# Optimization experiments

Hardware: AMD Instinct MI355X
Metric: run time of the kernel (lower is better)

## Reference

```python
import jax, jax.numpy as jnp
import numpy as np

H = 8  # n_head
EPS = 1e-5


def layernorm(x, g, b):
    m = jnp.mean(x, -1, keepdims=True)
    v = jnp.mean((x - m) ** 2, -1, keepdims=True)
    return (x - m) * jax.lax.rsqrt(v + EPS) * g + b


def setup_inputs() -> dict:
    key = jax.random.key(0)
    ks = jax.random.split(key, 32)
    b, t, d, f, n_mem, l_mem = 4, 256, 512, 2048, 64, 128
    sd = 1.0 / np.sqrt(d)
    sf = 1.0 / np.sqrt(f)
    rn = lambda k, shape, s: jax.random.normal(k, shape, jnp.float32) * s
    inp = {
        'dec_output': rn(ks[0], (b, t, d), 1.0),
        'tgt_mask': jnp.ones((b, t), dtype=bool),
        'mem_attn_out': rn(ks[1], (b, t, n_mem + 1), 1.0),
        'enc_out_mem': rn(ks[2], (n_mem, l_mem, d), 1.0),
        'tgt_emb_mem': rn(ks[3], (n_mem, l_mem, d), 1.0),
        'tgt_mask_mem': jnp.ones((n_mem, l_mem), dtype=bool),
        # MultiHeadedAttention params
        'Wq': rn(ks[4], (d, d), sd), 'bq': jnp.zeros((d,)),
        'Wk': rn(ks[5], (d, d), sd), 'bk': jnp.zeros((d,)),
        'Wv': rn(ks[6], (d, d), sd), 'bv': jnp.zeros((d,)),
        'Wo': rn(ks[7], (d, d), sd), 'bo': jnp.zeros((d,)),
        # LayerNorms (norms[0] pre, norms[1] post)
        'g0': jnp.ones((d,)), 'be0': jnp.zeros((d,)),
        'g1': jnp.ones((d,)), 'be1': jnp.zeros((d,)),
        # pos_ffn (applied to attended tokens)
        'W1': rn(ks[8], (d, f), sd), 'bf1': jnp.zeros((f,)),
        'W2': rn(ks[9], (f, d), sf), 'bf2': jnp.zeros((d,)),
        # pos_ffn2 (applied to all tokens at the end)
        'W3': rn(ks[10], (d, f), sd), 'bf3': jnp.zeros((f,)),
        'W4': rn(ks[11], (f, d), sf), 'bf4': jnp.zeros((d,)),
    }
    return inp


def reference(dec_output, tgt_mask, mem_attn_out, enc_out_mem, tgt_emb_mem, tgt_mask_mem,
              Wq, bq, Wk, bk, Wv, bv, Wo, bo, g0, be0, g1, be1,
              W1, bf1, W2, bf2, W3, bf3, W4, bf4):
    b, t, d = dec_output.shape
    dh = d // H
    x = layernorm(dec_output, g0, be0)                       # norms[0]

    samples = jnp.argmax(mem_attn_out, -1) - 1               # [b,t], -1 => no memory
    valid = samples >= 0
    s = jnp.clip(samples, 0, None)                           # safe gather index

    # Per-token gather of the selected memory entry (irregular access).
    K = enc_out_mem[s]                                       # [b,t,l_mem,d]
    V = tgt_emb_mem[s]                                       # [b,t,l_mem,d]
    kmask = tgt_mask_mem[s]                                  # [b,t,l_mem] True=valid

    # Single-row attention: token (b,t) queries memory entry samples[b,t].
    q = (x @ Wq + bq).reshape(b, t, H, dh)
    k = (K @ Wk + bk).reshape(b, t, -1, H, dh)
    v = (V @ Wv + bv).reshape(b, t, -1, H, dh)
    scores = jnp.einsum('bthd,btlhd->bthl', q, k) / np.sqrt(dh)
    scores = jnp.where(kmask[:, :, None, :], scores, -1e9)
    attn = jax.nn.softmax(scores, axis=-1)
    ctx = jnp.einsum('bthl,btlhd->bthd', attn, v).reshape(b, t, d)
    st = ctx @ Wo + bo + x                                   # residual = query

    # pos_ffn (residual) then norms[1]
    st = st + jax.nn.relu(st @ W1 + bf1) @ W2 + bf2
    st = layernorm(st, g1, be1)

    # scatter-back: zero for tokens with sample == -1
    x = x + jnp.where(valid[..., None], st, 0.0)

    # pos_ffn2 (residual)
    out = x + jax.nn.relu(x @ W3 + bf3) @ W4 + bf4
    return out
```

## Files before the change

kernel.cpp:

```cpp
#include <hip/hip_runtime.h>
#include <hip/hip_bf16.h>
#include <math.h>

#define DD    512
#define FF    2048
#define NMEM  64
#define LMEM  128
#define NH    8
#define DH    64
#define NTOK  1024
#define NMROW 8192

typedef __attribute__((ext_vector_type(4))) float f32x4;
typedef __attribute__((ext_vector_type(8))) short bf16x8;

__device__ inline unsigned short f2b(float f) {
    union { float f; unsigned int i; } u; u.f = f;
    unsigned int r = u.i + 0x7FFFu + ((u.i >> 16) & 1u);
    return (unsigned short)(r >> 16);
}
__device__ inline float b2f(unsigned short b) {
    union { unsigned int i; float f; } u; u.i = ((unsigned int)b) << 16;
    return u.f;
}
__device__ __forceinline__ void gload_lds(const void* src, void* dst) {
    __builtin_amdgcn_global_load_lds((const __attribute__((address_space(1))) void*)src,
        (__attribute__((address_space(3))) void*)dst, 16, 0, 0);
}

struct WSeg { const float* src; unsigned short* dst; int K, N, tile0; };

struct PrepArgs {
    const float4 *enc, *emb; ushort4 *encb, *embb;
    WSeg s[3];
    const float *mem_attn;
    int *samples, *blist, *bstart;
    const float *dec, *g0, *be0;
    float *x; unsigned short *xb, *ctxb;
};

__global__ __launch_bounds__(256)
void prep_kernel(PrepArgs a) {
    __shared__ float ld[32][33];
    __shared__ float red[8];
    __shared__ int ibuf[64 + 65 + 64];
    int b = blockIdx.x, tid = threadIdx.x;
    if (b < 4096) {
        int i = b * 256 + tid;
        float4 va = a.enc[i];
        a.encb[i] = make_ushort4(f2b(va.x), f2b(va.y), f2b(va.z), f2b(va.w));
        float4 vb = a.emb[i];
        a.embb[i] = make_ushort4(f2b(vb.x), f2b(vb.y), f2b(vb.z), f2b(vb.w));
        return;
    }
    if (b < 4864) {
        int t = b - 4096;
        int si = 0;
#pragma unroll
        for (int i = 1; i < 3; ++i) if (t >= a.s[i].tile0) si = i;
        const float* src = a.s[si].src;
        unsigned short* dst = a.s[si].dst;
        int K = a.s[si].K, N = a.s[si].N;
        int lt = t - a.s[si].tile0;
        int ntn = N >> 5;
        int k0 = (lt / ntn) << 5, n0 = (lt % ntn) << 5;
        int r = tid >> 3, c = (tid & 7) << 2;
        float4 v = *(const float4*)(src + (size_t)(k0 + r) * N + n0 + c);
        ld[r][c] = v.x; ld[r][c + 1] = v.y; ld[r][c + 2] = v.z; ld[r][c + 3] = v.w;
        __syncthreads();
        ushort4 o = make_ushort4(f2b(ld[c][r]), f2b(ld[c + 1][r]),
                                 f2b(ld[c + 2][r]), f2b(ld[c + 3][r]));
        *(ushort4*)(dst + (size_t)(n0 + r) * K + k0 + c) = o;
        return;
    }
    if (b < 5888) {
        int row = b - 4864;
        const float* xr = a.dec + (size_t)row * DD;
        float v0 = xr[tid], v1 = xr[tid + 256];
        float s = v0 + v1, s2 = v0 * v0 + v1 * v1;
        for (int off = 32; off > 0; off >>= 1) {
            s  += __shfl_down(s,  off, 64);
            s2 += __shfl_down(s2, off, 64);
        }
        int wave = tid >> 6, lane = tid & 63;
        if (lane == 0) { red[wave] = s; red[4 + wave] = s2; }
        __syncthreads();
        float S  = red[0] + red[1] + red[2] + red[3];
        float S2 = red[4] + red[5] + red[6] + red[7];
        float mean = S / (float)DD;
        float inv  = rsqrtf(S2 / (float)DD - mean * mean + 1e-5f);
        float o0 = (v0 - mean) * inv * a.g0[tid]       + a.be0[tid];
        float o1 = (v1 - mean) * inv * a.g0[tid + 256] + a.be0[tid + 256];
        size_t base = (size_t)row * DD;
        a.x[base + tid] = o0; a.x[base + tid + 256] = o1;
        a.xb[base + tid] = f2b(o0); a.xb[base + tid + 256] = f2b(o1);
        ((unsigned*)a.ctxb)[row * 256 + tid] = 0u;
        return;
    }
    int* scnt  = ibuf;
    int* soff  = ibuf + 64;
    int* scnt2 = ibuf + 129;
    if (tid < 64) { scnt[tid] = 0; scnt2[tid] = 0; }
    __syncthreads();
    int mys[4];
#pragma unroll
    for (int k = 0; k < 4; ++k) {
        int t = k * 256 + tid;
        const float* r = a.mem_attn + (size_t)t * (NMEM + 1);
        float best = r[0]; int bi = 0;
        for (int i = 1; i < NMEM + 1; ++i) {
            float v = r[i];
            if (v > best) { best = v; bi = i; }
        }
        int s = bi - 1;
        a.samples[t] = s; mys[k] = s;
        if (s >= 0) atomicAdd(&scnt[s], 1);
    }
    __syncthreads();
    if (tid == 0) {
        int run = 0;
        for (int e = 0; e < 64; ++e) { soff[e] = run; run += scnt[e]; }
        soff[64] = run;
    }
    __syncthreads();
    if (tid < 65) a.bstart[tid] = soff[tid];
#pragma unroll
    for (int k = 0; k < 4; ++k) {
        int t = k * 256 + tid;
        int s = mys[k];
        if (s >= 0) {
            int pos = soff[s] + atomicAdd(&scnt2[s], 1);
            a.blist[pos] = t;
        }
    }
}

__global__ __launch_bounds__(256)
void ln_scatter_kernel(const float* __restrict__ st2, const float* __restrict__ g,
                       const float* __restrict__ be, const float* __restrict__ x,
                       const int* __restrict__ samples, float* __restrict__ x2,
                       unsigned short* __restrict__ x2b) {
    int row = blockIdx.x;
    const float* xr = st2 + (size_t)row * DD;
    int tid = threadIdx.x;
    float v0 = xr[tid], v1 = xr[tid + 256];
    float s = v0 + v1, s2 = v0 * v0 + v1 * v1;
    for (int off = 32; off > 0; off >>= 1) {
        s  += __shfl_down(s,  off, 64);
        s2 += __shfl_down(s2, off, 64);
    }
    __shared__ float red[8];
    int wave = tid >> 6, lane = tid & 63;
    if (lane == 0) { red[wave] = s; red[4 + wave] = s2; }
    __syncthreads();
    float S  = red[0] + red[1] + red[2] + red[3];
    float S2 = red[4] + red[5] + red[6] + red[7];
    float mean = S / (float)DD;
    float inv  = rsqrtf(S2 / (float)DD - mean * mean + 1e-5f);
    float valid = (samples[row] >= 0) ? 1.f : 0.f;
    size_t base = (size_t)row * DD;
    float l0 = (v0 - mean) * inv * g[tid]       + be[tid];
    float l1 = (v1 - mean) * inv * g[tid + 256] + be[tid + 256];
    float r0 = x[base + tid]       + valid * l0;
    float r1 = x[base + tid + 256] + valid * l1;
    x2[base + tid] = r0; x2[base + tid + 256] = r1;
    x2b[base + tid] = f2b(r0); x2b[base + tid + 256] = f2b(r1);
}

template<int MI, int NI, int BK>
__device__ __forceinline__
void gemm_core(const unsigned short* __restrict__ A, const unsigned short* __restrict__ Bt,
               const float* __restrict__ bias, const float* __restrict__ res,
               float* __restrict__ C, unsigned short* __restrict__ Cb,
               int N, int K, int relu, int bx, int by,
               unsigned short* As0, unsigned short* As1,
               unsigned short* Bs0, unsigned short* Bs1) {
    constexpr int BM = MI * 32, BN = NI * 32;
    constexpr int CPR = BK / 8;
    constexpr int RB  = BK * 2;
    static_assert((BM * CPR + BN * CPR) / 256 == 8 || BK == 512, "8 loads/wave/tile");
    const int tid = threadIdx.x;
    const int lane = tid & 63, w = tid >> 6;
    const int wm = (w >> 1) * (MI * 16), wn = (w & 1) * (NI * 16);
    const int m0 = by * BM, n0 = bx * BN;
    f32x4 acc[MI][NI] = {};

    auto stage = [&](unsigned short* As, unsigned short* Bs, int k0) {
#pragma unroll
        for (int it = 0; it < BM * CPR / 256; ++it) {
            int f = it * 256 + tid;
            int row = f / CPR, ch = f % CPR;
            int sch = ch ^ (row & 7);
            gload_lds((const char*)(A + (size_t)(m0 + row) * K + k0) + sch * 16,
                      (char*)As + f * 16);
        }
#pragma unroll
        for (int it = 0; it < BN * CPR / 256; ++it) {
            int f = it * 256 + tid;
            int row = f / CPR, ch = f % CPR;
            int sch = ch ^ (row & 7);
            gload_lds((const char*)(Bt + (size_t)(n0 + row) * K + k0) + sch * 16,
                      (char*)Bs + f * 16);
        }
    };

    const int nt = K / BK;
    stage(As0, Bs0, 0);
    if (nt > 1) stage(As1, Bs1, BK);
    for (int t = 0; t < nt; ++t) {
        if (t + 1 < nt) {
            asm volatile("s_waitcnt vmcnt(8)" ::: "memory");
        } else {
            asm volatile("s_waitcnt vmcnt(0)" ::: "memory");
        }
        __builtin_amdgcn_s_barrier();
        __builtin_amdgcn_sched_barrier(0);
        const unsigned short* As = (t & 1) ? As1 : As0;
        const unsigned short* Bs = (t & 1) ? Bs1 : Bs0;
#pragma unroll
        for (int kk = 0; kk < BK / 32; ++kk) {
            bf16x8 af[MI], bfr[NI];
#pragma unroll
            for (int mi = 0; mi < MI; ++mi) {
                int row = wm + mi * 16 + (lane & 15);
                int ch = kk * 4 + (lane >> 4);
                af[mi] = *(const bf16x8*)((const char*)As + row * RB + ((ch ^ (row & 7)) * 16));
            }
#pragma unroll
            for (int ni = 0; ni < NI; ++ni) {
                int row = wn + ni * 16 + (lane & 15);
                int ch = kk * 4 + (lane >> 4);
                bfr[ni] = *(const bf16x8*)((const char*)Bs + row * RB + ((ch ^ (row & 7)) * 16));
            }
#pragma unroll
            for (int mi = 0; mi < MI; ++mi)
#pragma unroll
                for (int ni = 0; ni < NI; ++ni)
                    acc[mi][ni] = __builtin_amdgcn_mfma_f32_16x16x32_bf16(af[mi], bfr[ni], acc[mi][ni], 0, 0, 0);
        }
        __builtin_amdgcn_s_barrier();
        if (t + 2 < nt)
            stage((t & 1) ? As1 : As0, (t & 1) ? Bs1 : Bs0, (t + 2) * BK);
    }
#pragma unroll
    for (int mi = 0; mi < MI; ++mi) {
#pragma unroll
        for (int ni = 0; ni < NI; ++ni) {
            int col = n0 + wn + ni * 16 + (lane & 15);
            float bv = bias[col];
#pragma unroll
            for (int j = 0; j < 4; ++j) {
                int row = m0 + wm + mi * 16 + (lane >> 4) * 4 + j;
                size_t idx = (size_t)row * N + col;
                float v = acc[mi][ni][j] + bv;
                if (res)  v += res[idx];
                if (relu) v = fmaxf(v, 0.f);
                if (C)  C[idx] = v;
                if (Cb) Cb[idx] = f2b(v);
            }
        }
    }
}

template<int MI, int NI, int BK, int RELU>
__global__ __launch_bounds__(256)
void gemm_kernel(const unsigned short* __restrict__ A, const unsigned short* __restrict__ Bt,
                 const float* __restrict__ bias, const float* __restrict__ res,
                 float* __restrict__ C, unsigned short* __restrict__ Cb, int N, int K) {
    __shared__ __align__(16) unsigned short As0[MI * 32 * BK], As1[MI * 32 * BK];
    __shared__ __align__(16) unsigned short Bs0[NI * 32 * BK], Bs1[NI * 32 * BK];
    gemm_core<MI, NI, BK>(A, Bt, bias, res, C, Cb, N, K, RELU, blockIdx.x, blockIdx.y,
                          As0, As1, Bs0, Bs1);
}

template<int MI, int NI, int BK, int RELU>
__global__ __launch_bounds__(256)
void gemm1_kernel(const unsigned short* __restrict__ A, const unsigned short* __restrict__ Bt,
                  const float* __restrict__ bias, const float* __restrict__ res,
                  float* __restrict__ C, unsigned short* __restrict__ Cb, int N) {
    __shared__ __align__(16) unsigned short As[MI * 32 * BK];
    __shared__ __align__(16) unsigned short Bs[NI * 32 * BK];
    gemm_core<MI, NI, BK>(A, Bt, bias, res, C, Cb, N, BK, RELU, blockIdx.x, blockIdx.y,
                          As, As, Bs, Bs);
}

struct WSeg5s { WSeg s[5]; };

__global__ __launch_bounds__(256)
void attn_fused_kernel(const unsigned short* __restrict__ encb,
                       const unsigned short* __restrict__ embb,
                       const unsigned short* __restrict__ xb,
                       const unsigned short* __restrict__ WkT,
                       const unsigned short* __restrict__ WvT,
                       const unsigned short* __restrict__ WqT,
                       const float* __restrict__ bk, const float* __restrict__ bv,
                       const float* __restrict__ bq,
                       const int* __restrict__ blist, const int* __restrict__ bstart,
                       unsigned short* __restrict__ ctxb, WSeg5s wsegs) {
    __shared__ __align__(16) unsigned short As[128 * 64];
    __shared__ __align__(16) unsigned short Ws[64 * 64];
    __shared__ __align__(16) unsigned short Ks[128 * 64];
    __shared__ __align__(16) unsigned short Vt[64 * 128];
    __shared__ float qsb[32 * 64];
    __shared__ float ps[2][128];
    __shared__ float red[8];
    __shared__ int toks[32];
    const int b = blockIdx.x, tid = threadIdx.x;
    const int lane = tid & 63, w = tid >> 6;

    if (b >= 512) {
        float* ld = (float*)As;
#pragma unroll 1
        for (int j = 0; j < 8; ++j) {
            int t = (b - 512) * 8 + j;
            int si = 0;
#pragma unroll
            for (int i = 1; i < 5; ++i) if (t >= wsegs.s[i].tile0) si = i;
            const float* src = wsegs.s[si].src;
            unsigned short* dst = wsegs.s[si].dst;
            int K = wsegs.s[si].K, N = wsegs.s[si].N;
            int lt = t - wsegs.s[si].tile0;
            int ntn = N >> 5;
            int k0 = (lt / ntn) << 5, n0 = (lt % ntn) << 5;
            int r = tid >> 3, c = (tid & 7) << 2;
            float4 v = *(const float4*)(src + (size_t)(k0 + r) * N + n0 + c);
            ld[r * 33 + c] = v.x; ld[r * 33 + c + 1] = v.y;
            ld[r * 33 + c + 2] = v.z; ld[r * 33 + c + 3] = v.w;
            __syncthreads();
            ushort4 o = make_ushort4(f2b(ld[c * 33 + r]), f2b(ld[(c + 1) * 33 + r]),
                                     f2b(ld[(c + 2) * 33 + r]), f2b(ld[(c + 3) * 33 + r]));
            *(ushort4*)(dst + (size_t)(n0 + r) * K + k0 + c) = o;
            __syncthreads();
        }
        return;
    }

    const int e = b & 63, h = b >> 6;
    const int beg = bstart[e], end = bstart[e + 1];
    if (end <= beg) return;

#pragma unroll 1
    for (int ph = 0; ph < 2; ++ph) {
        const unsigned short* Am = (ph ? embb : encb) + (size_t)e * LMEM * DD;
        const unsigned short* Wm = (ph ? WvT : WkT) + (size_t)h * DH * DD;
        const float* bias = ph ? bv : bk;
        f32x4 acc[2][4] = {};
        for (int k0 = 0; k0 < DD; k0 += 64) {
            __syncthreads();
#pragma unroll
            for (int it = 0; it < 4; ++it) {
                int f = it * 256 + tid;
                int row = f >> 3, ch = f & 7, sch = ch ^ (row & 7);
                gload_lds((const char*)(Am + (size_t)row * DD + k0) + sch * 16,
                          (char*)As + f * 16);
            }
#pragma unroll
            for (int it = 0; it < 2; ++it) {
                int f = it * 256 + tid;
                int row = f >> 3, ch = f & 7, sch = ch ^ (row & 7);
                gload_lds((const char*)(Wm + (size_t)row * DD + k0) + sch * 16,
                          (char*)Ws + f * 16);
            }
            __syncthreads();
#pragma unroll
            for (int kk = 0; kk < 2; ++kk) {
                int ch = kk * 4 + (lane >> 4);
                bf16x8 af[2], bfr[4];
#pragma unroll
                for (int mi = 0; mi < 2; ++mi) {
                    int row = w * 32 + mi * 16 + (lane & 15);
                    af[mi] = *(const bf16x8*)((const char*)As + row * 128 + ((ch ^ (row & 7)) * 16));
                }
#pragma unroll
                for (int ni = 0; ni < 4; ++ni) {
                    int row = ni * 16 + (lane & 15);
                    bfr[ni] = *(const bf16x8*)((const char*)Ws + row * 128 + ((ch ^ (row & 7)) * 16));
                }
#pragma unroll
                for (int mi = 0; mi < 2; ++mi)
#pragma unroll
                    for (int ni = 0; ni < 4; ++ni)
                        acc[mi][ni] = __builtin_amdgcn_mfma_f32_16x16x32_bf16(af[mi], bfr[ni], acc[mi][ni], 0, 0, 0);
            }
        }
#pragma unroll
        for (int mi = 0; mi < 2; ++mi) {
#pragma unroll
            for (int ni = 0; ni < 4; ++ni) {
                int d = ni * 16 + (lane & 15);
                float bvv = bias[h * DH + d];
#pragma unroll
                for (int j = 0; j < 4; ++j) {
                    int l = w * 32 + mi * 16 + (lane >> 4) * 4 + j;
                    unsigned short val = f2b(acc[mi][ni][j] + bvv);
                    if (ph == 0) {
                        int c = d >> 3;
                        *(unsigned short*)((char*)Ks + l * 128 + ((c ^ (l & 7)) * 16) + (d & 7) * 2) = val;
                    } else {
                        int cc = l >> 3;
                        int slot = (cc & 8) | ((cc ^ d) & 7);
                        *(unsigned short*)((char*)Vt + d * 256 + slot * 16 + (l & 7) * 2) = val;
                    }
                }
            }
        }
    }

    const int sub = tid >> 7, lt = tid & 127;
    for (int g0 = beg; g0 < end; g0 += 32) {
        int gcnt = end - g0; if (gcnt > 32) gcnt = 32;
        __syncthreads();
        if (tid < 32) toks[tid] = blist[(g0 + tid < end) ? (g0 + tid) : (end - 1)];
        f32x4 qacc[2] = {};
        for (int k0 = 0; k0 < DD; k0 += 64) {
            __syncthreads();
            {
                int row = tid >> 3, ch = tid & 7, sch = ch ^ (row & 7);
                gload_lds((const char*)(xb + (size_t)toks[row] * DD + k0) + sch * 16,
                          (char*)As + tid * 16);
            }
#pragma unroll
            for (int it = 0; it < 2; ++it) {
                int f = it * 256 + tid;
                int row = f >> 3, ch = f & 7, sch = ch ^ (row & 7);
                gload_lds((const char*)(WqT + (size_t)(h * DH + row) * DD + k0) + sch * 16,
                          (char*)Ws + f * 16);
            }
            __syncthreads();
#pragma unroll
            for (int kk = 0; kk < 2; ++kk) {
                int ch = kk * 4 + (lane >> 4);
                int ar = (w >> 1) * 16 + (lane & 15);
                bf16x8 af = *(const bf16x8*)((const char*)As + ar * 128 + ((ch ^ (ar & 7)) * 16));
#pragma unroll
                for (int ni = 0; ni < 2; ++ni) {
                    int br = (w & 1) * 32 + ni * 16 + (lane & 15);
                    bf16x8 bfr = *(const bf16x8*)((const char*)Ws + br * 128 + ((ch ^ (br & 7)) * 16));
                    qacc[ni] = __builtin_amdgcn_mfma_f32_16x16x32_bf16(af, bfr, qacc[ni], 0, 0, 0);
                }
            }
        }
#pragma unroll
        for (int ni = 0; ni < 2; ++ni)
#pragma unroll
            for (int j = 0; j < 4; ++j) {
                int r = (w >> 1) * 16 + (lane >> 4) * 4 + j;
                int d = (w & 1) * 32 + ni * 16 + (lane & 15);
                qsb[r * 64 + d] = qacc[ni][j] + bq[h * DH + d];
            }
        __syncthreads();

        int iters = (gcnt + 1) >> 1;
        for (int it = 0; it < iters; ++it) {
            int tl = it * 2 + sub;
            float sc = 0.f;
#pragma unroll
            for (int c = 0; c < 8; ++c) {
                bf16x8 kv = *(const bf16x8*)((char*)Ks + lt * 128 + ((c ^ (lt & 7)) * 16));
#pragma unroll
                for (int j = 0; j < 8; ++j) sc = fmaf(qsb[tl * 64 + c * 8 + j], b2f((unsigned short)kv[j]), sc);
            }
            sc *= 0.125f;
            float mx = sc;
            for (int off = 32; off > 0; off >>= 1) mx = fmaxf(mx, __shfl_xor(mx, off, 64));
            if ((tid & 63) == 0) red[tid >> 6] = mx;
            __syncthreads();
            mx = fmaxf(red[sub * 2], red[sub * 2 + 1]);
            float ex = __expf(sc - mx);
            float sm = ex;
            for (int off = 32; off > 0; off >>= 1) sm += __shfl_xor(sm, off, 64);
            if ((tid & 63) == 0) red[4 + (tid >> 6)] = sm;
            __syncthreads();
            sm = red[4 + sub * 2] + red[4 + sub * 2 + 1];
            ps[sub][lt] = ex / sm;
            __syncthreads();
            if (tid < 128) {
                int sub2 = tid >> 6, d = tid & 63;
                int tl2 = it * 2 + sub2;
                if (g0 + tl2 < end) {
                    int tok2 = toks[tl2];
                    float acc2 = 0.f;
#pragma unroll
                    for (int cc = 0; cc < 16; ++cc) {
                        int slot = (cc & 8) | ((cc ^ d) & 7);
                        bf16x8 vv = *(const bf16x8*)((char*)Vt + d * 256 + slot * 16);
#pragma unroll
                        for (int j = 0; j < 8; ++j) acc2 = fmaf(ps[sub2][cc * 8 + j], b2f((unsigned short)vv[j]), acc2);
                    }
                    ctxb[(size_t)tok2 * DD + h * DH + d] = f2b(acc2);
                }
            }
            __syncthreads();
        }
    }
}

extern "C" void kernel_launch(void* const* d_in, const int* in_sizes, int n_in,
                              void* d_out, int out_size, void* d_ws, size_t ws_size,
                              hipStream_t stream) {
    const float* dec      = (const float*)d_in[0];
    const float* mem_attn = (const float*)d_in[2];
    const float* enc_mem  = (const float*)d_in[3];
    const float* emb_mem  = (const float*)d_in[4];
    const float* Wq = (const float*)d_in[6];  const float* bq = (const float*)d_in[7];
    const float* Wk = (const float*)d_in[8];  const float* bk = (const float*)d_in[9];
    const float* Wv = (const float*)d_in[10]; const float* bv = (const float*)d_in[11];
    const float* Wo = (const float*)d_in[12]; const float* bo = (const float*)d_in[13];
    const float* g0 = (const float*)d_in[14]; const float* be0 = (const float*)d_in[15];
    const float* g1 = (const float*)d_in[16]; const float* be1 = (const float*)d_in[17];
    const float* W1 = (const float*)d_in[18]; const float* bf1 = (const float*)d_in[19];
    const float* W2 = (const float*)d_in[20]; const float* bf2 = (const float*)d_in[21];
    const float* W3 = (const float*)d_in[22]; const float* bf3 = (const float*)d_in[23];
    const float* W4 = (const float*)d_in[24]; const float* bf4 = (const float*)d_in[25];
    float* out = (float*)d_out;

    const size_t MB = 1u << 20;
    char* ws = (char*)d_ws;
    unsigned short* encb  = (unsigned short*)(ws + 0 * MB);
    unsigned short* embb  = (unsigned short*)(ws + 8 * MB);
    unsigned short* WqT = (unsigned short*)(ws + 32 * MB);
    unsigned short* WkT = (unsigned short*)(ws + 32 * MB + 512 * 1024);
    unsigned short* WvT = (unsigned short*)(ws + 33 * MB);
    unsigned short* WoT = (unsigned short*)(ws + 33 * MB + 512 * 1024);
    unsigned short* W1T = (unsigned short*)(ws + 34 * MB);
    unsigned short* W2T = (unsigned short*)(ws + 36 * MB);
    unsigned short* W3T = (unsigned short*)(ws + 38 * MB);
    unsigned short* W4T = (unsigned short*)(ws + 40 * MB);
    float*          x    = (float*)(ws + 42 * MB);
    unsigned short* xb   = (unsigned short*)(ws + 44 * MB);
    unsigned short* ctxb = (unsigned short*)(ws + 47 * MB);
    int*         samples = (int*)(ws + 48 * MB);
    int*         blist   = (int*)(ws + 48 * MB + 4096);
    int*         bstart  = (int*)(ws + 48 * MB + 8192);
    float*          st   = (float*)(ws + 0 * MB);
    unsigned short* stb  = (unsigned short*)(ws + 2 * MB);
    unsigned short* h1b  = (unsigned short*)(ws + 3 * MB);
    float*          st2  = (float*)(ws + 8 * MB);
    float*          x2   = (float*)(ws + 10 * MB);
    unsigned short* x2b  = (unsigned short*)(ws + 12 * MB);
    unsigned short* h2b  = (unsigned short*)(ws + 13 * MB);

    PrepArgs pa;
    pa.enc = (const float4*)enc_mem; pa.emb = (const float4*)emb_mem;
    pa.encb = (ushort4*)encb; pa.embb = (ushort4*)embb;
    pa.s[0] = { Wq, WqT, DD, DD,   0 };
    pa.s[1] = { Wk, WkT, DD, DD, 256 };
    pa.s[2] = { Wv, WvT, DD, DD, 512 };
    pa.mem_attn = mem_attn; pa.samples = samples; pa.blist = blist; pa.bstart = bstart;
    pa.dec = dec; pa.g0 = g0; pa.be0 = be0;
    pa.x = x; pa.xb = xb; pa.ctxb = ctxb;
    prep_kernel<<<5889, 256, 0, stream>>>(pa);
    WSeg5s wt;
    wt.s[0] = { Wo, WoT, DD, DD,    0 };
    wt.s[1] = { W1, W1T, DD, FF,  256 };
    wt.s[2] = { W2, W2T, FF, DD, 1280 };
    wt.s[3] = { W3, W3T, DD, FF, 2304 };
    wt.s[4] = { W4, W4T, FF, DD, 3328 };
    attn_fused_kernel<<<512 + 544, 256, 0, stream>>>(encb, embb, xb, WkT, WvT, WqT,
                                                     bk, bv, bq, blist, bstart, ctxb, wt);
    gemm1_kernel<1,1,512,0><<<dim3(16, 32), 256, 0, stream>>>(ctxb, WoT, bo, x, st, stb, DD);
    gemm_kernel<2,2,128,1><<<dim3(32, 16), 256, 0, stream>>>(stb, W1T, bf1, nullptr, nullptr, h1b, FF, DD);
    gemm_kernel<1,1,256,0><<<dim3(16, 32), 256, 0, stream>>>(h1b, W2T, bf2, st, st2, nullptr, DD, FF);
    ln_scatter_kernel<<<NTOK, 256, 0, stream>>>(st2, g1, be1, x, samples, x2, x2b);
    gemm_kernel<2,2,128,1><<<dim3(32, 16), 256, 0, stream>>>(x2b, W3T, bf3, nullptr, nullptr, h2b, FF, DD);
    gemm_kernel<1,1,256,0><<<dim3(16, 32), 256, 0, stream>>>(h2b, W4T, bf4, x2, out, nullptr, DD, FF);
}
```

Baseline: 122.4 us.

## Use MFMA for memory attention scores and context, load K/V projection operands directly

Replaces the per-token scalar FMA score and context loops in the fused memory-attention kernel with bf16 MFMA tiles over 32 tokens at once, using a block-wide softmax reduction through shared memory. The K/V and Q projection GEMMs now read operands straight from global memory into registers instead of staging them through LDS, which frees shared memory. It also adds a launch-bounds occupancy hint. Scores and probabilities are rounded to bf16, which slightly reduces precision, and dropping LDS staging relies on the cache for operand reuse.

```diff
diff --git a/kernel.cpp b/kernel.cpp
--- a/kernel.cpp
+++ b/kernel.cpp
@@ -286,7 +286,7 @@
 
 struct WSeg5s { WSeg s[5]; };
 
-__global__ __launch_bounds__(256)
+__global__ __launch_bounds__(256, 3)
 void attn_fused_kernel(const unsigned short* __restrict__ encb,
                        const unsigned short* __restrict__ embb,
                        const unsigned short* __restrict__ xb,
@@ -297,19 +297,17 @@
                        const float* __restrict__ bq,
                        const int* __restrict__ blist, const int* __restrict__ bstart,
                        unsigned short* __restrict__ ctxb, WSeg5s wsegs) {
-    __shared__ __align__(16) unsigned short As[128 * 64];
-    __shared__ __align__(16) unsigned short Ws[64 * 64];
     __shared__ __align__(16) unsigned short Ks[128 * 64];
     __shared__ __align__(16) unsigned short Vt[64 * 128];
-    __shared__ float qsb[32 * 64];
-    __shared__ float ps[2][128];
-    __shared__ float red[8];
+    __shared__ __align__(16) unsigned short Qs[32 * 64];
+    __shared__ __align__(16) unsigned short Ps[32 * 128];
+    __shared__ float redm[2][32], reds[2][32];
     __shared__ int toks[32];
     const int b = blockIdx.x, tid = threadIdx.x;
     const int lane = tid & 63, w = tid >> 6;
 
     if (b >= 512) {
-        float* ld = (float*)As;
+        float* ld = (float*)Ks;
 #pragma unroll 1
         for (int j = 0; j < 8; ++j) {
             int t = (b - 512) * 8 + j;
@@ -341,47 +339,25 @@
 
 #pragma unroll 1
     for (int ph = 0; ph < 2; ++ph) {
-        const unsigned short* Am = (ph ? embb : encb) + (size_t)e * LMEM * DD;
-        const unsigned short* Wm = (ph ? WvT : WkT) + (size_t)h * DH * DD;
+        const unsigned short* Am = (ph ? embb : encb) + (size_t)e * (LMEM * DD);
+        const unsigned short* Wm = (ph ? WvT : WkT) + (size_t)h * (DH * DD);
         const float* bias = ph ? bv : bk;
         f32x4 acc[2][4] = {};
-        for (int k0 = 0; k0 < DD; k0 += 64) {
-            __syncthreads();
-#pragma unroll
-            for (int it = 0; it < 4; ++it) {
-                int f = it * 256 + tid;
-                int row = f >> 3, ch = f & 7, sch = ch ^ (row & 7);
-                gload_lds((const char*)(Am + (size_t)row * DD + k0) + sch * 16,
-                          (char*)As + f * 16);
-            }
-#pragma unroll
-            for (int it = 0; it < 2; ++it) {
-                int f = it * 256 + tid;
-                int row = f >> 3, ch = f & 7, sch = ch ^ (row & 7);
-                gload_lds((const char*)(Wm + (size_t)row * DD + k0) + sch * 16,
-                          (char*)Ws + f * 16);
-            }
-            __syncthreads();
-#pragma unroll
-            for (int kk = 0; kk < 2; ++kk) {
-                int ch = kk * 4 + (lane >> 4);
-                bf16x8 af[2], bfr[4];
-#pragma unroll
-                for (int mi = 0; mi < 2; ++mi) {
-                    int row = w * 32 + mi * 16 + (lane & 15);
-                    af[mi] = *(const bf16x8*)((const char*)As + row * 128 + ((ch ^ (row & 7)) * 16));
-                }
-#pragma unroll
-                for (int ni = 0; ni < 4; ++ni) {
-                    int row = ni * 16 + (lane & 15);
-                    bfr[ni] = *(const bf16x8*)((const char*)Ws + row * 128 + ((ch ^ (row & 7)) * 16));
-                }
-#pragma unroll
-                for (int mi = 0; mi < 2; ++mi)
-#pragma unroll
-                    for (int ni = 0; ni < 4; ++ni)
-                        acc[mi][ni] = __builtin_amdgcn_mfma_f32_16x16x32_bf16(af[mi], bfr[ni], acc[mi][ni], 0, 0, 0);
-            }
+        const unsigned short* ar0 = Am + (size_t)(w * 32 + (lane & 15)) * DD + (lane >> 4) * 8;
+        const unsigned short* br0 = Wm + (size_t)(lane & 15) * DD + (lane >> 4) * 8;
+#pragma unroll 4
+        for (int ks = 0; ks < 16; ++ks) {
+            bf16x8 af[2], bfr[4];
+            af[0] = *(const bf16x8*)(ar0 + ks * 32);
+            af[1] = *(const bf16x8*)(ar0 + 16 * DD + ks * 32);
+#pragma unroll
+            for (int ni = 0; ni < 4; ++ni)
+                bfr[ni] = *(const bf16x8*)(br0 + (size_t)ni * 16 * DD + ks * 32);
+#pragma unroll
+            for (int mi = 0; mi < 2; ++mi)
+#pragma unroll
+                for (int ni = 0; ni < 4; ++ni)
+                    acc[mi][ni] = __builtin_amdgcn_mfma_f32_16x16x32_bf16(af[mi], bfr[ni], acc[mi][ni], 0, 0, 0);
         }
 #pragma unroll
         for (int mi = 0; mi < 2; ++mi) {
@@ -405,92 +381,122 @@
             }
         }
     }
-
-    const int sub = tid >> 7, lt = tid & 127;
+    __syncthreads();
+
+    const int m = w & 1, nh = w >> 1;
     for (int g0 = beg; g0 < end; g0 += 32) {
-        int gcnt = end - g0; if (gcnt > 32) gcnt = 32;
         __syncthreads();
         if (tid < 32) toks[tid] = blist[(g0 + tid < end) ? (g0 + tid) : (end - 1)];
-        f32x4 qacc[2] = {};
-        for (int k0 = 0; k0 < DD; k0 += 64) {
-            __syncthreads();
-            {
-                int row = tid >> 3, ch = tid & 7, sch = ch ^ (row & 7);
-                gload_lds((const char*)(xb + (size_t)toks[row] * DD + k0) + sch * 16,
-                          (char*)As + tid * 16);
-            }
-#pragma unroll
-            for (int it = 0; it < 2; ++it) {
-                int f = it * 256 + tid;
-                int row = f >> 3, ch = f & 7, sch = ch ^ (row & 7);
-                gload_lds((const char*)(WqT + (size_t)(h * DH + row) * DD + k0) + sch * 16,
-                          (char*)Ws + f * 16);
-            }
-            __syncthreads();
-#pragma unroll
-            for (int kk = 0; kk < 2; ++kk) {
-                int ch = kk * 4 + (lane >> 4);
-                int ar = (w >> 1) * 16 + (lane & 15);
-                bf16x8 af = *(const bf16x8*)((const char*)As + ar * 128 + ((ch ^ (ar & 7)) * 16));
+        __syncthreads();
+        {
+            int tokr = toks[m * 16 + (lane & 15)];
+            const unsigned short* ar = xb + (size_t)tokr * DD + (lane >> 4) * 8;
+            const unsigned short* br = WqT + (size_t)(h * DH + nh * 32 + (lane & 15)) * DD + (lane >> 4) * 8;
+            f32x4 qacc[2] = {};
+#pragma unroll 4
+            for (int ks = 0; ks < 16; ++ks) {
+                bf16x8 aq = *(const bf16x8*)(ar + ks * 32);
 #pragma unroll
                 for (int ni = 0; ni < 2; ++ni) {
-                    int br = (w & 1) * 32 + ni * 16 + (lane & 15);
-                    bf16x8 bfr = *(const bf16x8*)((const char*)Ws + br * 128 + ((ch ^ (br & 7)) * 16));
-                    qacc[ni] = __builtin_amdgcn_mfma_f32_16x16x32_bf16(af, bfr, qacc[ni], 0, 0, 0);
+                    bf16x8 b8 = *(const bf16x8*)(br + (size_t)ni * 16 * DD + ks * 32);
+                    qacc[ni] = __builtin_amdgcn_mfma_f32_16x16x32_bf16(aq, b8, qacc[ni], 0, 0, 0);
                 }
             }
-        }
-#pragma unroll
-        for (int ni = 0; ni < 2; ++ni)
+#pragma unroll
+            for (int ni = 0; ni < 2; ++ni) {
+                int d = nh * 32 + ni * 16 + (lane & 15);
+                float bqv = bq[h * DH + d];
+                int ch = d >> 3;
+#pragma unroll
+                for (int j = 0; j < 4; ++j) {
+                    int r = m * 16 + (lane >> 4) * 4 + j;
+                    *(unsigned short*)((char*)Qs + r * 128 + ((ch ^ (r & 7)) * 16) + (d & 7) * 2)
+                        = f2b((qacc[ni][j] + bqv) * 0.125f);
+                }
+            }
+        }
+        __syncthreads();
+        f32x4 sacc[4] = {};
+#pragma unroll
+        for (int kk = 0; kk < 2; ++kk) {
+            int ch = kk * 4 + (lane >> 4);
+            int ra = m * 16 + (lane & 15);
+            bf16x8 aq = *(const bf16x8*)((char*)Qs + ra * 128 + ((ch ^ (ra & 7)) * 16));
+#pragma unroll
+            for (int nt = 0; nt < 4; ++nt) {
+                int rk = nh * 64 + nt * 16 + (lane & 15);
+                bf16x8 k8 = *(const bf16x8*)((char*)Ks + rk * 128 + ((ch ^ (rk & 7)) * 16));
+                sacc[nt] = __builtin_amdgcn_mfma_f32_16x16x32_bf16(aq, k8, sacc[nt], 0, 0, 0);
+            }
+        }
+        float mj[4];
+#pragma unroll
+        for (int j = 0; j < 4; ++j)
+            mj[j] = fmaxf(fmaxf(sacc[0][j], sacc[1][j]), fmaxf(sacc[2][j], sacc[3][j]));
+#pragma unroll
+        for (int off = 1; off < 16; off <<= 1)
+#pragma unroll
+            for (int j = 0; j < 4; ++j) mj[j] = fmaxf(mj[j], __shfl_xor(mj[j], off, 64));
+        if ((lane & 15) == 0)
+#pragma unroll
+            for (int j = 0; j < 4; ++j) redm[nh][m * 16 + (lane >> 4) * 4 + j] = mj[j];
+        __syncthreads();
+        float ex[4][4], sj[4];
+#pragma unroll
+        for (int j = 0; j < 4; ++j) {
+            int r = m * 16 + (lane >> 4) * 4 + j;
+            float mx = fmaxf(redm[0][r], redm[1][r]);
+            sj[j] = 0.f;
+#pragma unroll
+            for (int nt = 0; nt < 4; ++nt) {
+                ex[nt][j] = __expf(sacc[nt][j] - mx);
+                sj[j] += ex[nt][j];
+            }
+        }
+#pragma unroll
+        for (int off = 1; off < 16; off <<= 1)
+#pragma unroll
+            for (int j = 0; j < 4; ++j) sj[j] += __shfl_xor(sj[j], off, 64);
+        if ((lane & 15) == 0)
+#pragma unroll
+            for (int j = 0; j < 4; ++j) reds[nh][m * 16 + (lane >> 4) * 4 + j] = sj[j];
+        __syncthreads();
+#pragma unroll
+        for (int j = 0; j < 4; ++j) {
+            int r = m * 16 + (lane >> 4) * 4 + j;
+            float inv = 1.f / (reds[0][r] + reds[1][r]);
+#pragma unroll
+            for (int nt = 0; nt < 4; ++nt) {
+                int c = nh * 64 + nt * 16 + (lane & 15);
+                int cc = c >> 3;
+                *(unsigned short*)((char*)Ps + r * 256 + ((cc ^ (r & 7)) * 16) + (c & 7) * 2)
+                    = f2b(ex[nt][j] * inv);
+            }
+        }
+        __syncthreads();
+        f32x4 cacc[2] = {};
+#pragma unroll
+        for (int kk = 0; kk < 4; ++kk) {
+            int cc = kk * 4 + (lane >> 4);
+            int rp = m * 16 + (lane & 15);
+            bf16x8 ap = *(const bf16x8*)((char*)Ps + rp * 256 + ((cc ^ (rp & 7)) * 16));
+#pragma unroll
+            for (int ni = 0; ni < 2; ++ni) {
+                int d = nh * 32 + ni * 16 + (lane & 15);
+                int slot = (cc & 8) | ((cc ^ d) & 7);
+                bf16x8 v8 = *(const bf16x8*)((char*)Vt + d * 256 + slot * 16);
+                cacc[ni] = __builtin_amdgcn_mfma_f32_16x16x32_bf16(ap, v8, cacc[ni], 0, 0, 0);
+            }
+        }
+#pragma unroll
+        for (int ni = 0; ni < 2; ++ni) {
+            int d = nh * 32 + ni * 16 + (lane & 15);
 #pragma unroll
             for (int j = 0; j < 4; ++j) {
-                int r = (w >> 1) * 16 + (lane >> 4) * 4 + j;
-                int d = (w & 1) * 32 + ni * 16 + (lane & 15);
-                qsb[r * 64 + d] = qacc[ni][j] + bq[h * DH + d];
-            }
-        __syncthreads();
-
-        int iters = (gcnt + 1) >> 1;
-        for (int it = 0; it < iters; ++it) {
-            int tl = it * 2 + sub;
-            float sc = 0.f;
-#pragma unroll
-            for (int c = 0; c < 8; ++c) {
-                bf16x8 kv = *(const bf16x8*)((char*)Ks + lt * 128 + ((c ^ (lt & 7)) * 16));
-#pragma unroll
-                for (int j = 0; j < 8; ++j) sc = fmaf(qsb[tl * 64 + c * 8 + j], b2f((unsigned short)kv[j]), sc);
-            }
-            sc *= 0.125f;
-            float mx = sc;
-            for (int off = 32; off > 0; off >>= 1) mx = fmaxf(mx, __shfl_xor(mx, off, 64));
-            if ((tid & 63) == 0) red[tid >> 6] = mx;
-            __syncthreads();
-            mx = fmaxf(red[sub * 2], red[sub * 2 + 1]);
-            float ex = __expf(sc - mx);
-            float sm = ex;
-            for (int off = 32; off > 0; off >>= 1) sm += __shfl_xor(sm, off, 64);
-            if ((tid & 63) == 0) red[4 + (tid >> 6)] = sm;
-            __syncthreads();
-            sm = red[4 + sub * 2] + red[4 + sub * 2 + 1];
-            ps[sub][lt] = ex / sm;
-            __syncthreads();
-            if (tid < 128) {
-                int sub2 = tid >> 6, d = tid & 63;
-                int tl2 = it * 2 + sub2;
-                if (g0 + tl2 < end) {
-                    int tok2 = toks[tl2];
-                    float acc2 = 0.f;
-#pragma unroll
-                    for (int cc = 0; cc < 16; ++cc) {
-                        int slot = (cc & 8) | ((cc ^ d) & 7);
-                        bf16x8 vv = *(const bf16x8*)((char*)Vt + d * 256 + slot * 16);
-#pragma unroll
-                        for (int j = 0; j < 8; ++j) acc2 = fmaf(ps[sub2][cc * 8 + j], b2f((unsigned short)vv[j]), acc2);
-                    }
-                    ctxb[(size_t)tok2 * DD + h * DH + d] = f2b(acc2);
-                }
-            }
-            __syncthreads();
+                int r = m * 16 + (lane >> 4) * 4 + j;
+                if (g0 + r < end)
+                    ctxb[(size_t)toks[r] * DD + h * DH + d] = f2b(cacc[ni][j]);
+            }
         }
     }
 }
```

New measurement: 130.8 us. 6.9% more time.

## Assign one wavefront per token in memory attention, removing block barriers

Applied to the files above, without the earlier changes.

Each wavefront now handles one token's single-row attention over all 128 memory keys (two keys per lane). Query and probability values are broadcast with readlane instead of through shared memory, and the softmax reductions are done only with intra-wave shuffles. This removes the per-token-pair __syncthreads and the LDS staging of probabilities, and keeps all four waves busy in the PV step where only two were used before. The trade-off is more readlane and scalar work per FMA, and each wave now does the full 128-key dot product on its own.

```diff
diff --git a/kernel.cpp b/kernel.cpp
--- a/kernel.cpp
+++ b/kernel.cpp
@@ -302,8 +302,6 @@
     __shared__ __align__(16) unsigned short Ks[128 * 64];
     __shared__ __align__(16) unsigned short Vt[64 * 128];
     __shared__ float qsb[32 * 64];
-    __shared__ float ps[2][128];
-    __shared__ float red[8];
     __shared__ int toks[32];
     const int b = blockIdx.x, tid = threadIdx.x;
     const int lane = tid & 63, w = tid >> 6;
@@ -406,7 +404,6 @@
         }
     }
 
-    const int sub = tid >> 7, lt = tid & 127;
     for (int g0 = beg; g0 < end; g0 += 32) {
         int gcnt = end - g0; if (gcnt > 32) gcnt = 32;
         __syncthreads();
@@ -450,47 +447,44 @@
             }
         __syncthreads();
 
-        int iters = (gcnt + 1) >> 1;
-        for (int it = 0; it < iters; ++it) {
-            int tl = it * 2 + sub;
-            float sc = 0.f;
+        for (int tl = w; tl < gcnt; tl += 4) {
+            int token = toks[tl];
+            float qv = qsb[tl * 64 + lane];
+            int qb = __float_as_int(qv);
+            float sc0 = 0.f, sc1 = 0.f;
 #pragma unroll
             for (int c = 0; c < 8; ++c) {
-                bf16x8 kv = *(const bf16x8*)((char*)Ks + lt * 128 + ((c ^ (lt & 7)) * 16));
-#pragma unroll
-                for (int j = 0; j < 8; ++j) sc = fmaf(qsb[tl * 64 + c * 8 + j], b2f((unsigned short)kv[j]), sc);
-            }
-            sc *= 0.125f;
-            float mx = sc;
+                bf16x8 k0v = *(const bf16x8*)((char*)Ks + lane * 128 + ((c ^ (lane & 7)) * 16));
+                bf16x8 k1v = *(const bf16x8*)((char*)Ks + (lane + 64) * 128 + ((c ^ (lane & 7)) * 16));
+#pragma unroll
+                for (int j = 0; j < 8; ++j) {
+                    float qd = __int_as_float(__builtin_amdgcn_readlane(qb, c * 8 + j));
+                    sc0 = fmaf(qd, b2f((unsigned short)k0v[j]), sc0);
+                    sc1 = fmaf(qd, b2f((unsigned short)k1v[j]), sc1);
+                }
+            }
+            sc0 *= 0.125f; sc1 *= 0.125f;
+            float mx = fmaxf(sc0, sc1);
             for (int off = 32; off > 0; off >>= 1) mx = fmaxf(mx, __shfl_xor(mx, off, 64));
-            if ((tid & 63) == 0) red[tid >> 6] = mx;
-            __syncthreads();
-            mx = fmaxf(red[sub * 2], red[sub * 2 + 1]);
-            float ex = __expf(sc - mx);
-            float sm = ex;
+            float p0 = __expf(sc0 - mx), p1 = __expf(sc1 - mx);
+            float sm = p0 + p1;
             for (int off = 32; off > 0; off >>= 1) sm += __shfl_xor(sm, off, 64);
-            if ((tid & 63) == 0) red[4 + (tid >> 6)] = sm;
-            __syncthreads();
-            sm = red[4 + sub * 2] + red[4 + sub * 2 + 1];
-            ps[sub][lt] = ex / sm;
-            __syncthreads();
-            if (tid < 128) {
-                int sub2 = tid >> 6, d = tid & 63;
-                int tl2 = it * 2 + sub2;
-                if (g0 + tl2 < end) {
-                    int tok2 = toks[tl2];
-                    float acc2 = 0.f;
-#pragma unroll
-                    for (int cc = 0; cc < 16; ++cc) {
-                        int slot = (cc & 8) | ((cc ^ d) & 7);
-                        bf16x8 vv = *(const bf16x8*)((char*)Vt + d * 256 + slot * 16);
-#pragma unroll
-                        for (int j = 0; j < 8; ++j) acc2 = fmaf(ps[sub2][cc * 8 + j], b2f((unsigned short)vv[j]), acc2);
-                    }
-                    ctxb[(size_t)tok2 * DD + h * DH + d] = f2b(acc2);
+            float inv = 1.f / sm;
+            int p0b = __float_as_int(p0 * inv), p1b = __float_as_int(p1 * inv);
+            float acc2 = 0.f;
+            const int d = lane;
+#pragma unroll
+            for (int cc = 0; cc < 16; ++cc) {
+                int slot = (cc & 8) | ((cc ^ d) & 7);
+                bf16x8 vv = *(const bf16x8*)((char*)Vt + d * 256 + slot * 16);
+#pragma unroll
+                for (int j = 0; j < 8; ++j) {
+                    int l = cc * 8 + j;
+                    float pl = __int_as_float(__builtin_amdgcn_readlane(l < 64 ? p0b : p1b, l & 63));
+                    acc2 = fmaf(pl, b2f((unsigned short)vv[j]), acc2);
                 }
             }
-            __syncthreads();
+            ctxb[(size_t)token * DD + h * DH + d] = f2b(acc2);
         }
     }
 }
```

Result: slower. 144.8 us (+18.3%).
